# Kernel optimization log

Measured on AMD Instinct MI355X. Metric: run time of the kernel, lower is better.

The kernel has to match this reference:

```python
import jax, jax.numpy as jnp
import numpy as np

THETA = 10.0      # spike threshold
TAU_SR = 1.0      # SRM (psp) kernel time constant
TAU_REF = 1.0     # refractory kernel time constant
SCALE_REF = 2.0   # refractory kernel scale (SLAYER default: -2*theta peak)


@jax.custom_vjp
def spike_fn(v):
    # Heaviside on (membrane - theta); surrogate gradient in bwd (SLAYER-style pdf)
    return (v >= 0.0).astype(v.dtype)

def _spike_fwd(v):
    return spike_fn(v), v

def _spike_bwd(v, g):
    return (g * jnp.exp(-jnp.abs(v) / THETA) / THETA,)

spike_fn.defvjp(_spike_fwd, _spike_bwd)


def alpha_psp(x, tau):
    """Causal conv of x (T, B, F) with alpha kernel eps[k] = (k/tau)*exp(1-k/tau),
    implemented as a 2-state linear recurrence (exact for the discrete kernel)."""
    d = jnp.float32(np.exp(-1.0 / tau))
    c = jnp.float32(np.e / tau)

    def step(carry, xt):
        p, q = carry
        q = d * (q + p)          # q[t] = sum_s x[s]*(t-s)*d^(t-s)
        p = d * p + xt           # p[t] = sum_s x[s]*d^(t-s)
        return (p, q), c * q

    z = jnp.zeros_like(x[0])
    _, out = jax.lax.scan(step, (z, z), x)
    return out


def spike_dyn(u, tau_ref, scale_ref, theta):
    """Threshold-with-refractory dynamics. u: (T, B, F) synaptic drive.
    membrane[t] = u[t] - scale_ref*theta * (alpha refractory conv of past spikes)."""
    d = jnp.float32(np.exp(-1.0 / tau_ref))
    c = jnp.float32(np.e / tau_ref)
    cref = jnp.float32(-scale_ref * theta) * c

    def step(carry, ut):
        p, q = carry
        q = d * (q + p)                       # refractory trace (lag-0 coeff is 0)
        s = spike_fn(ut + cref * q - theta)   # spike if membrane >= theta
        p = d * p + s
        return (p, q), s

    z = jnp.zeros_like(u[0])
    _, s = jax.lax.scan(step, (z, z), u)
    return s


def setup_inputs() -> dict:
    key = jax.random.key(0)
    k1, k2, k3 = jax.random.split(key, 3)
    # sparse binary input spike trains, (B, C, H, W, T) SLAYER layout
    downsampled = (jax.random.uniform(k1, (16, 2, 50, 63, 500)) < 0.1).astype(jnp.float32)
    w1 = jax.random.normal(k2, (1024, 6300), dtype=jnp.float32) * 0.1
    w2 = jax.random.normal(k3, (20, 1024), dtype=jnp.float32) * 0.1
    return {"downsampled": downsampled, "w1": w1, "w2": w2}


def reference(downsampled, w1, w2):
    B, T = downsampled.shape[0], downsampled.shape[-1]
    x = downsampled.reshape(B, -1, T).transpose(2, 0, 1)   # (T, B, 6300)
    p1 = alpha_psp(x, TAU_SR)                              # psp filter
    u1 = jnp.einsum('tbf,of->tbo', p1, w1)                 # fc1 (per-timestep dense)
    s1 = spike_dyn(u1, TAU_REF, SCALE_REF, THETA)          # spike layer 1
    p2 = alpha_psp(s1, TAU_SR)
    u2 = jnp.einsum('tbh,oh->tbo', p2, w2)                 # fc2
    s2 = spike_dyn(u2, TAU_REF, SCALE_REF, THETA)
    return s2.transpose(1, 2, 0)                           # (B, output_size, T)
```

## Files before the change

### kernel.cpp

```cpp
#include <hip/hip_runtime.h>
#include <cstdint>
#include <cstddef>

#define T_N   500
#define B_N   16
#define F_IN  6300
#define KW    198
#define KPAD  6336
#define H1    1024
#define H2    20
#define N2P   32
#define M_N   8000
#define M_PADN 8064

#define DD_C   0.36787944117144233f
#define CC_C   2.718281828459045f
#define THETA_C 10.0f
#define INV2048 4.8828125e-4f

typedef _Float16 half8 __attribute__((ext_vector_type(8)));
typedef __attribute__((ext_vector_type(4))) float f32x4;

__device__ __forceinline__ unsigned short f2h_bits(float x) {
    union { _Float16 h; unsigned short u; } c; c.h = (_Float16)x; return c.u;
}
__device__ __forceinline__ float h2f(unsigned short u) {
    union { _Float16 h; unsigned short u; } c; c.u = u; return (float)c.h;
}

__global__ void prep_fused_k(const float* __restrict__ x,
                             const float* __restrict__ w1,
                             const float* __restrict__ w2,
                             uint32_t* __restrict__ bits_t,
                             unsigned short* __restrict__ w1f,
                             unsigned short* __restrict__ w2f) {
    const int bid = blockIdx.x;
    if (bid < 6336) {
        const int b    = bid & 15;
        const int tmp  = bid >> 4;
        const int w    = tmp % 198;
        const int tch2 = tmp / 198;
        const int t    = tch2 * 256 + threadIdx.x;
        if (t >= 504) return;
        const int m = t * 16 + b;
        uint32_t word = 0u;
        if (t < T_N) {
            const int fbase = w * 32;
            #pragma unroll
            for (int j = 0; j < 32; ++j) {
                const int f = fbase + j;
                float v = 0.f;
                if (f < F_IN) v = x[((size_t)b * F_IN + f) * T_N + t];
                word |= (v != 0.f ? 1u : 0u) << j;
            }
        }
        bits_t[(size_t)w * M_PADN + m] = word;
    } else if (bid < 6336 + 1024) {
        const int o = bid - 6336;
        #pragma unroll 1
        for (int it = 0; it < 25; ++it) {
            const int f = it * 256 + threadIdx.x;
            if (f >= KPAD) break;
            float w = (f < F_IN) ? w1[(size_t)o * F_IN + f] : 0.f;
            const unsigned short h1 = f2h_bits(w);
            const float r1 = w - h2f(h1);
            const unsigned short h2 = f2h_bits(r1 * 2048.0f);
            const size_t base = (size_t)o * KPAD + f;
            w1f[base]                     = h1;
            w1f[(size_t)H1 * KPAD + base] = h2;
        }
    } else {
        const int o = bid - 7360;
        #pragma unroll
        for (int it = 0; it < 4; ++it) {
            const int k = it * 256 + threadIdx.x;
            float w = (o < H2) ? w2[(size_t)o * H1 + k] : 0.f;
            const unsigned short h1 = f2h_bits(w);
            const float r1 = w - h2f(h1);
            const unsigned short h2 = f2h_bits(r1 * 2048.0f);
            const size_t base = (size_t)o * H1 + k;
            w2f[base]                    = h1;
            w2f[(size_t)N2P * H1 + base] = h2;
        }
    }
}

__global__ __launch_bounds__(256, 2)
void gemm1_mfma_k(const uint32_t* __restrict__ bits_t,
                  const unsigned short* __restrict__ w1f,
                  float* __restrict__ u1) {
    __shared__ uint32_t BsU[2][2 * 128 * 16];

    const int tid  = threadIdx.x;
    const int lane = tid & 63;
    const int wave = tid >> 6;
    const int wr = wave >> 1, wc = wave & 1;
    const int n0 = blockIdx.x * 128;
    const int m0 = blockIdx.y * 128;
    const int l15 = lane & 15, g = lane >> 4;

    const unsigned short* bsrc0 =
        w1f + (size_t)(n0 + (lane >> 2)) * KPAD + ((lane & 3) ^ ((lane >> 3) & 3)) * 8;

    const uint32_t* pbits = bits_t + m0 + wr * 64 + l15;

    f32x4 acc[2][4][4];
    const f32x4 fz = {0.f, 0.f, 0.f, 0.f};
    #pragma unroll
    for (int t = 0; t < 2; ++t)
        #pragma unroll
        for (int i = 0; i < 4; ++i)
            #pragma unroll
            for (int j = 0; j < 4; ++j) acc[t][i][j] = fz;

    int boff[4];
    #pragma unroll
    for (int ni = 0; ni < 4; ++ni) {
        const int br = wc * 64 + ni * 16 + l15;
        boff[ni] = br * 16 + ((g ^ ((br >> 1) & 3)) << 2);
    }

#define STAGE_B(tt, bb)                                                        \
    {                                                                          \
        _Pragma("unroll")                                                      \
        for (int j = 0; j < 4; ++j) {                                          \
            const int e    = wave * 4 + j;                                     \
            const int term = e >> 3;                                           \
            const int ii   = e & 7;                                            \
            const unsigned short* src =                                        \
                bsrc0 + (size_t)(term * H1 + ii * 16) * KPAD + (size_t)(tt) * 32; \
            __builtin_amdgcn_global_load_lds(                                  \
                (const __attribute__((address_space(1))) uint32_t*)src,        \
                (__attribute__((address_space(3))) uint32_t*)&BsU[bb][term * 2048 + ii * 256], \
                16, 0, 0);                                                     \
        }                                                                      \
    }

#define LOAD_W(W, tt)                                                          \
    {                                                                          \
        _Pragma("unroll")                                                      \
        for (int mi = 0; mi < 4; ++mi)                                         \
            W[mi] = pbits[(size_t)(tt) * M_PADN + mi * 16];                    \
    }

#define COMPUTE(W, bb)                                                         \
    {                                                                          \
        half8 af[4];                                                           \
        _Pragma("unroll")                                                      \
        for (int mi = 0; mi < 4; ++mi) {                                       \
            union { uint32_t u[4]; half8 h; } cv;                              \
            _Pragma("unroll")                                                  \
            for (int i = 0; i < 4; ++i) {                                      \
                const int b0 = g * 8 + 2 * i;                                  \
                cv.u[i] = (((W[mi] >> b0) & 1u) ? 0x00003C00u : 0u) |          \
                          (((W[mi] >> (b0 + 1)) & 1u) ? 0x3C000000u : 0u);     \
            }                                                                  \
            af[mi] = cv.h;                                                     \
        }                                                                      \
        __builtin_amdgcn_s_setprio(1);                                         \
        _Pragma("unroll")                                                      \
        for (int term = 0; term < 2; ++term) {                                 \
            half8 bfv[4];                                                      \
            _Pragma("unroll")                                                  \
            for (int ni = 0; ni < 4; ++ni)                                     \
                bfv[ni] = *(const half8*)&BsU[bb][term * 2048 + boff[ni]];     \
            _Pragma("unroll")                                                  \
            for (int mi = 0; mi < 4; ++mi)                                     \
                _Pragma("unroll")                                              \
                for (int ni = 0; ni < 4; ++ni)                                 \
                    acc[term][mi][ni] = __builtin_amdgcn_mfma_f32_16x16x32_f16( \
                        af[mi], bfv[ni], acc[term][mi][ni], 0, 0, 0);          \
        }                                                                      \
        __builtin_amdgcn_s_setprio(0);                                         \
    }

#define ITER(tt, cb, WCUR, WNEXT)                                              \
    {                                                                          \
        LOAD_W(WNEXT, (tt) + 1);                                               \
        STAGE_B((tt) + 1, (cb) ^ 1);                                           \
        COMPUTE(WCUR, cb);                                                     \
        __syncthreads();                                                       \
    }

    uint32_t wA[4], wB[4];
    LOAD_W(wA, 0);
    STAGE_B(0, 0);
    __syncthreads();

    for (int t = 0; t < KW - 2; t += 2) {
        ITER(t,     0, wA, wB);
        ITER(t + 1, 1, wB, wA);
    }
    ITER(KW - 2, 0, wA, wB);
    COMPUTE(wB, 1);

#undef ITER
#undef COMPUTE
#undef LOAD_W
#undef STAGE_B

    #pragma unroll
    for (int mi = 0; mi < 4; ++mi) {
        const int mbase = m0 + wr * 64 + mi * 16 + g * 4;
        #pragma unroll
        for (int ni = 0; ni < 4; ++ni) {
            const int o = n0 + wc * 64 + ni * 16 + l15;
            #pragma unroll
            for (int r = 0; r < 4; ++r)
                u1[(size_t)(mbase + r) * H1 + o] =
                    acc[0][mi][ni][r] + acc[1][mi][ni][r] * INV2048;
        }
    }
}

__global__ void scan1_k(const float* __restrict__ u1, unsigned short* __restrict__ s1f) {
    const int lane = blockIdx.x * 64 + threadIdx.x;
    const float CREF = -20.0f * CC_C;
    float p1 = 0.f, q1 = 0.f, pr = 0.f, qr = 0.f;
    float A[10], Bv[10];

#define STEP1(xv, tidx) {                                   \
        q1 = DD_C * (q1 + p1); p1 = DD_C * p1 + (xv);       \
        const float uu = CC_C * q1;                         \
        qr = DD_C * (qr + pr);                              \
        const float vv = uu + CREF * qr - THETA_C;          \
        const float ss = (vv >= 0.f) ? 1.f : 0.f;           \
        pr = DD_C * pr + ss;                                \
        s1f[(size_t)(tidx) * 16384 + lane] =                \
            (vv >= 0.f) ? (unsigned short)0x3C00 : (unsigned short)0; }

    #pragma unroll
    for (int j = 0; j < 10; ++j) A[j] = u1[(size_t)j * 16384 + lane];
    for (int it = 0; it < 25; ++it) {
        const int gB = 2 * it + 1;
        #pragma unroll
        for (int j = 0; j < 10; ++j) Bv[j] = u1[(size_t)(gB * 10 + j) * 16384 + lane];
        #pragma unroll
        for (int j = 0; j < 10; ++j) STEP1(A[j], (2 * it) * 10 + j);
        if (it < 24) {
            const int gA = 2 * it + 2;
            #pragma unroll
            for (int j = 0; j < 10; ++j) A[j] = u1[(size_t)(gA * 10 + j) * 16384 + lane];
        }
        #pragma unroll
        for (int j = 0; j < 10; ++j) STEP1(Bv[j], gB * 10 + j);
    }
#undef STEP1
}

__global__ __launch_bounds__(256)
void gemm2_mfma_k(const unsigned short* __restrict__ s1f,
                  const unsigned short* __restrict__ w2f,
                  float* __restrict__ u2p) {
    __shared__ uint32_t AsU[128 * 16];
    __shared__ uint32_t BsU[2 * 32 * 16];

    const int tid  = threadIdx.x;
    const int lane = tid & 63;
    const int wave = tid >> 6;
    const int m0 = blockIdx.x * 128;
    const int kc = blockIdx.y;
    const int l15 = lane & 15, g = lane >> 4;

    f32x4 acc[2][2][2];
    const f32x4 fz = {0.f, 0.f, 0.f, 0.f};
    #pragma unroll
    for (int t = 0; t < 2; ++t)
        #pragma unroll
        for (int i = 0; i < 2; ++i)
            #pragma unroll
            for (int j = 0; j < 2; ++j) acc[t][i][j] = fz;

    int aoff[2], boff[2][2];
    #pragma unroll
    for (int mi = 0; mi < 2; ++mi) {
        const int ar = wave * 32 + mi * 16 + l15;
        aoff[mi] = ar * 16 + ((g ^ ((ar >> 1) & 3)) << 2);
    }
    #pragma unroll
    for (int term = 0; term < 2; ++term)
        #pragma unroll
        for (int ni = 0; ni < 2; ++ni) {
            const int br = ni * 16 + l15;
            boff[term][ni] = term * 512 + br * 16 + ((g ^ ((br >> 1) & 3)) << 2);
        }

    for (int kw8 = 0; kw8 < 8; ++kw8) {
        const int kw = kc * 8 + kw8;
        __syncthreads();
        #pragma unroll
        for (int i = 0; i < 2; ++i) {
            const int c   = i * 256 + tid;
            const int row = c >> 2;
            const int kch = c & 3;
            const unsigned short* src =
                s1f + (size_t)(m0 + row) * H1 + kw * 32 + (kch ^ ((row >> 1) & 3)) * 8;
            __builtin_amdgcn_global_load_lds(
                (const __attribute__((address_space(1))) uint32_t*)src,
                (__attribute__((address_space(3))) uint32_t*)&AsU[(i * 256 + wave * 64) * 4],
                16, 0, 0);
        }
        {
            const int c    = tid;
            const int term = c >> 7;
            const int o    = (c >> 2) & 31;
            const int kch  = c & 3;
            const unsigned short* src =
                w2f + (size_t)(term * N2P + o) * H1 + kw * 32 + (kch ^ ((o >> 1) & 3)) * 8;
            __builtin_amdgcn_global_load_lds(
                (const __attribute__((address_space(1))) uint32_t*)src,
                (__attribute__((address_space(3))) uint32_t*)&BsU[wave * 256],
                16, 0, 0);
        }
        __syncthreads();

        half8 af[2];
        #pragma unroll
        for (int mi = 0; mi < 2; ++mi) af[mi] = *(const half8*)&AsU[aoff[mi]];
        #pragma unroll
        for (int term = 0; term < 2; ++term)
            #pragma unroll
            for (int ni = 0; ni < 2; ++ni) {
                const half8 bf = *(const half8*)&BsU[boff[term][ni]];
                #pragma unroll
                for (int mi = 0; mi < 2; ++mi)
                    acc[term][mi][ni] = __builtin_amdgcn_mfma_f32_16x16x32_f16(
                        af[mi], bf, acc[term][mi][ni], 0, 0, 0);
            }
    }

    #pragma unroll
    for (int mi = 0; mi < 2; ++mi) {
        const int mbase = m0 + wave * 32 + mi * 16 + g * 4;
        #pragma unroll
        for (int ni = 0; ni < 2; ++ni) {
            const int o = ni * 16 + l15;
            #pragma unroll
            for (int r = 0; r < 4; ++r)
                u2p[((size_t)kc * M_PADN + mbase + r) * N2P + o] =
                    acc[0][mi][ni][r] + acc[1][mi][ni][r] * INV2048;
        }
    }
}

__global__ void scan2_k(const float* __restrict__ u2p, float* __restrict__ out) {
    const int lane = blockIdx.x * 64 + threadIdx.x;
    if (lane >= 320) return;
    const int b  = lane / 20;
    const int o2 = lane % 20;
    const int boffs = b * N2P + o2;
    const float CREF = -20.0f * CC_C;
    float p1 = 0.f, q1 = 0.f, pr = 0.f, qr = 0.f;
    float A[10], Bv[10];

#define LOAD2(tidx)                                                         \
    (u2p[(size_t)0 * M_PADN * N2P + (size_t)(tidx) * 512 + boffs] +         \
     u2p[(size_t)1 * M_PADN * N2P + (size_t)(tidx) * 512 + boffs] +         \
     u2p[(size_t)2 * M_PADN * N2P + (size_t)(tidx) * 512 + boffs] +         \
     u2p[(size_t)3 * M_PADN * N2P + (size_t)(tidx) * 512 + boffs])

#define STEP2(xv, tidx) {                                   \
        q1 = DD_C * (q1 + p1); p1 = DD_C * p1 + (xv);       \
        const float uu = CC_C * q1;                         \
        qr = DD_C * (qr + pr);                              \
        const float vv = uu + CREF * qr - THETA_C;          \
        const float ss = (vv >= 0.f) ? 1.f : 0.f;           \
        pr = DD_C * pr + ss;                                \
        out[(size_t)lane * T_N + (tidx)] = ss; }

    #pragma unroll
    for (int j = 0; j < 10; ++j) A[j] = LOAD2(j);
    for (int it = 0; it < 25; ++it) {
        const int gB = 2 * it + 1;
        #pragma unroll
        for (int j = 0; j < 10; ++j) Bv[j] = LOAD2(gB * 10 + j);
        #pragma unroll
        for (int j = 0; j < 10; ++j) STEP2(A[j], (2 * it) * 10 + j);
        if (it < 24) {
            const int gA = 2 * it + 2;
            #pragma unroll
            for (int j = 0; j < 10; ++j) A[j] = LOAD2(gA * 10 + j);
        }
        #pragma unroll
        for (int j = 0; j < 10; ++j) STEP2(Bv[j], gB * 10 + j);
    }
#undef STEP2
#undef LOAD2
}

extern "C" void kernel_launch(void* const* d_in, const int* in_sizes, int n_in,
                              void* d_out, int out_size, void* d_ws, size_t ws_size,
                              hipStream_t stream) {
    const float* x  = (const float*)d_in[0];
    const float* w1 = (const float*)d_in[1];
    const float* w2 = (const float*)d_in[2];
    float* out = (float*)d_out;

    char* ws = (char*)d_ws;
    size_t off = 0;
    uint32_t*       bits_t = (uint32_t*)(ws + off);       off += (size_t)KW * M_PADN * 4;
    unsigned short* w1f    = (unsigned short*)(ws + off); off += (size_t)2 * H1 * KPAD * 2;
    unsigned short* w2f    = (unsigned short*)(ws + off); off += (size_t)2 * N2P * H1 * 2;
    float*          u1     = (float*)(ws + off);          off += (size_t)M_PADN * H1 * 4;
    unsigned short* s1f    = (unsigned short*)(ws + off); off += (size_t)M_PADN * H1 * 2;
    float*          u2p    = (float*)(ws + off);          off += (size_t)4 * M_PADN * N2P * 4;
    (void)ws_size; (void)in_sizes; (void)n_in; (void)out_size;

    prep_fused_k  <<<7392,        256, 0, stream>>>(x, w1, w2, bits_t, w1f, w2f);
    gemm1_mfma_k  <<<dim3(8, 63), 256, 0, stream>>>(bits_t, w1f, u1);
    scan1_k       <<<256,         64,  0, stream>>>(u1, s1f);
    gemm2_mfma_k  <<<dim3(63, 4), 256, 0, stream>>>(s1f, w2f, u2p);
    scan2_k       <<<5,           64,  0, stream>>>(u2p, out);
}
```

Baseline: 349.1 us.

## Replace split-fp16 GEMM1 with three-plane int8 MFMA on binary spike inputs

GEMM1 previously multiplied binary spike masks by a two-term fp16 split of w1 using f16 MFMA. Now w1 is quantized into three int8 planes (scales 2^-7, 2^-14, 2^-21) and multiplied with 0/1 int8 activations using the i32 16x16x64 i8 MFMA, so each instruction covers twice the K depth. Activation bits are unpacked with a multiply-and-mask trick, and the spike bit words are re-laid out in pairs so one uint2 load covers a 64-wide K step. The wave tiling changes to 8x2 tiles per wave. The cost is a third weight plane and a different quantization error profile, which the thresholded spike output is sensitive to.

```diff
diff --git a/kernel.cpp b/kernel.cpp
--- a/kernel.cpp
+++ b/kernel.cpp
@@ -6,6 +6,7 @@
 #define B_N   16
 #define F_IN  6300
 #define KW    198
+#define NS64  99
 #define KPAD  6336
 #define H1    1024
 #define H2    20
@@ -18,8 +19,13 @@
 #define THETA_C 10.0f
 #define INV2048 4.8828125e-4f
 
+#define S1_C 0.0078125f
+#define S2_C 6.103515625e-5f
+#define S3_C 4.76837158203125e-7f
+
 typedef _Float16 half8 __attribute__((ext_vector_type(8)));
 typedef __attribute__((ext_vector_type(4))) float f32x4;
+typedef __attribute__((ext_vector_type(4))) int   i32x4;
 
 __device__ __forceinline__ unsigned short f2h_bits(float x) {
     union { _Float16 h; unsigned short u; } c; c.h = (_Float16)x; return c.u;
@@ -31,8 +37,8 @@
 __global__ void prep_fused_k(const float* __restrict__ x,
                              const float* __restrict__ w1,
                              const float* __restrict__ w2,
-                             uint32_t* __restrict__ bits_t,
-                             unsigned short* __restrict__ w1f,
+                             uint32_t* __restrict__ bits2,
+                             signed char* __restrict__ w1q,
                              unsigned short* __restrict__ w2f) {
     const int bid = blockIdx.x;
     if (bid < 6336) {
@@ -54,7 +60,7 @@
                 word |= (v != 0.f ? 1u : 0u) << j;
             }
         }
-        bits_t[(size_t)w * M_PADN + m] = word;
+        bits2[(size_t)(w >> 1) * (M_PADN * 2) + m * 2 + (w & 1)] = word;
     } else if (bid < 6336 + 1024) {
         const int o = bid - 6336;
         #pragma unroll 1
@@ -62,12 +68,16 @@
             const int f = it * 256 + threadIdx.x;
             if (f >= KPAD) break;
             float w = (f < F_IN) ? w1[(size_t)o * F_IN + f] : 0.f;
-            const unsigned short h1 = f2h_bits(w);
-            const float r1 = w - h2f(h1);
-            const unsigned short h2 = f2h_bits(r1 * 2048.0f);
+            const int q1 = __float2int_rn(w * 128.0f);
+            const float r1 = w - (float)q1 * S1_C;
+            const int q2 = __float2int_rn(r1 * 16384.0f);
+            const float r2 = r1 - (float)q2 * S2_C;
+            const int q3 = __float2int_rn(r2 * 2097152.0f);
             const size_t base = (size_t)o * KPAD + f;
-            w1f[base]                     = h1;
-            w1f[(size_t)H1 * KPAD + base] = h2;
+            const size_t PL = (size_t)H1 * KPAD;
+            w1q[base]          = (signed char)q1;
+            w1q[PL + base]     = (signed char)q2;
+            w1q[2 * PL + base] = (signed char)q3;
         }
     } else {
         const int o = bid - 7360;
@@ -86,129 +96,115 @@
 }
 
 __global__ __launch_bounds__(256, 2)
-void gemm1_mfma_k(const uint32_t* __restrict__ bits_t,
-                  const unsigned short* __restrict__ w1f,
-                  float* __restrict__ u1) {
-    __shared__ uint32_t BsU[2][2 * 128 * 16];
+void gemm1_i8_k(const uint32_t* __restrict__ bits2,
+                const signed char* __restrict__ w1q,
+                float* __restrict__ u1) {
+    __shared__ uint32_t BsU[2][12 * 512];
 
     const int tid  = threadIdx.x;
     const int lane = tid & 63;
     const int wave = tid >> 6;
-    const int wr = wave >> 1, wc = wave & 1;
     const int n0 = blockIdx.x * 128;
     const int m0 = blockIdx.y * 128;
     const int l15 = lane & 15, g = lane >> 4;
 
-    const unsigned short* bsrc0 =
-        w1f + (size_t)(n0 + (lane >> 2)) * KPAD + ((lane & 3) ^ ((lane >> 3) & 3)) * 8;
-
-    const uint32_t* pbits = bits_t + m0 + wr * 64 + l15;
-
-    f32x4 acc[2][4][4];
-    const f32x4 fz = {0.f, 0.f, 0.f, 0.f};
-    #pragma unroll
-    for (int t = 0; t < 2; ++t)
-        #pragma unroll
-        for (int i = 0; i < 4; ++i)
-            #pragma unroll
-            for (int j = 0; j < 4; ++j) acc[t][i][j] = fz;
-
-    int boff[4];
-    #pragma unroll
-    for (int ni = 0; ni < 4; ++ni) {
-        const int br = wc * 64 + ni * 16 + l15;
-        boff[ni] = br * 16 + ((g ^ ((br >> 1) & 3)) << 2);
-    }
-
-#define STAGE_B(tt, bb)                                                        \
+    const signed char* bbase = w1q + (size_t)(n0 + lane) * KPAD;
+    uint32_t boffg[6];
+    uint32_t bdst[6];
+    #pragma unroll
+    for (int j = 0; j < 6; ++j) {
+        const int e = wave * 6 + j, slab = e >> 1, h = e & 1;
+        const int t = slab >> 2, gg = slab & 3;
+        boffg[j] = (uint32_t)((t * H1 + h * 64) * KPAD + gg * 16);
+        bdst[j]  = (uint32_t)(slab * 512 + h * 256 + lane * 4);
+    }
+
+    const uint2* pb = (const uint2*)bits2 + (size_t)m0 + l15;
+    const uint32_t hi2 = (g & 2);
+    const uint32_t sh  = (g & 1) * 16;
+
+    uint32_t bfoff[6];
+    #pragma unroll
+    for (int t = 0; t < 3; ++t)
+        #pragma unroll
+        for (int ni = 0; ni < 2; ++ni)
+            bfoff[t * 2 + ni] = (uint32_t)((t * 4 + g) * 512 + (wave * 32 + ni * 16 + l15) * 4);
+
+    i32x4 acc[3][8][2];
+    #pragma unroll
+    for (int t = 0; t < 3; ++t)
+        #pragma unroll
+        for (int mi = 0; mi < 8; ++mi)
+            #pragma unroll
+            for (int ni = 0; ni < 2; ++ni) acc[t][mi][ni] = (i32x4){0, 0, 0, 0};
+
+#define STAGE(ss, bb)                                                          \
     {                                                                          \
         _Pragma("unroll")                                                      \
-        for (int j = 0; j < 4; ++j) {                                          \
-            const int e    = wave * 4 + j;                                     \
-            const int term = e >> 3;                                           \
-            const int ii   = e & 7;                                            \
-            const unsigned short* src =                                        \
-                bsrc0 + (size_t)(term * H1 + ii * 16) * KPAD + (size_t)(tt) * 32; \
+        for (int j = 0; j < 6; ++j) {                                          \
             __builtin_amdgcn_global_load_lds(                                  \
-                (const __attribute__((address_space(1))) uint32_t*)src,        \
-                (__attribute__((address_space(3))) uint32_t*)&BsU[bb][term * 2048 + ii * 256], \
+                (const __attribute__((address_space(1))) uint32_t*)            \
+                    (bbase + (size_t)boffg[j] + (size_t)(ss) * 64),            \
+                (__attribute__((address_space(3))) uint32_t*)&BsU[bb][bdst[j]],\
                 16, 0, 0);                                                     \
         }                                                                      \
     }
 
-#define LOAD_W(W, tt)                                                          \
-    {                                                                          \
-        _Pragma("unroll")                                                      \
-        for (int mi = 0; mi < 4; ++mi)                                         \
-            W[mi] = pbits[(size_t)(tt) * M_PADN + mi * 16];                    \
-    }
-
-#define COMPUTE(W, bb)                                                         \
-    {                                                                          \
-        half8 af[4];                                                           \
-        _Pragma("unroll")                                                      \
-        for (int mi = 0; mi < 4; ++mi) {                                       \
-            union { uint32_t u[4]; half8 h; } cv;                              \
-            _Pragma("unroll")                                                  \
-            for (int i = 0; i < 4; ++i) {                                      \
-                const int b0 = g * 8 + 2 * i;                                  \
-                cv.u[i] = (((W[mi] >> b0) & 1u) ? 0x00003C00u : 0u) |          \
-                          (((W[mi] >> (b0 + 1)) & 1u) ? 0x3C000000u : 0u);     \
-            }                                                                  \
-            af[mi] = cv.h;                                                     \
-        }                                                                      \
-        __builtin_amdgcn_s_setprio(1);                                         \
-        _Pragma("unroll")                                                      \
-        for (int term = 0; term < 2; ++term) {                                 \
-            half8 bfv[4];                                                      \
-            _Pragma("unroll")                                                  \
-            for (int ni = 0; ni < 4; ++ni)                                     \
-                bfv[ni] = *(const half8*)&BsU[bb][term * 2048 + boff[ni]];     \
-            _Pragma("unroll")                                                  \
-            for (int mi = 0; mi < 4; ++mi)                                     \
-                _Pragma("unroll")                                              \
-                for (int ni = 0; ni < 4; ++ni)                                 \
-                    acc[term][mi][ni] = __builtin_amdgcn_mfma_f32_16x16x32_f16( \
-                        af[mi], bfv[ni], acc[term][mi][ni], 0, 0, 0);          \
-        }                                                                      \
-        __builtin_amdgcn_s_setprio(0);                                         \
-    }
-
-#define ITER(tt, cb, WCUR, WNEXT)                                              \
-    {                                                                          \
-        LOAD_W(WNEXT, (tt) + 1);                                               \
-        STAGE_B((tt) + 1, (cb) ^ 1);                                           \
-        COMPUTE(WCUR, cb);                                                     \
-        __syncthreads();                                                       \
-    }
-
-    uint32_t wA[4], wB[4];
-    LOAD_W(wA, 0);
-    STAGE_B(0, 0);
+    const uint32_t MAGIC = 0x00204081u;
+    const uint32_t PICK  = 0x01010101u;
+
+    STAGE(0, 0);
     __syncthreads();
 
-    for (int t = 0; t < KW - 2; t += 2) {
-        ITER(t,     0, wA, wB);
-        ITER(t + 1, 1, wB, wA);
-    }
-    ITER(KW - 2, 0, wA, wB);
-    COMPUTE(wB, 1);
-
-#undef ITER
-#undef COMPUTE
-#undef LOAD_W
-#undef STAGE_B
-
-    #pragma unroll
-    for (int mi = 0; mi < 4; ++mi) {
-        const int mbase = m0 + wr * 64 + mi * 16 + g * 4;
-        #pragma unroll
-        for (int ni = 0; ni < 4; ++ni) {
-            const int o = n0 + wc * 64 + ni * 16 + l15;
-            #pragma unroll
-            for (int r = 0; r < 4; ++r)
-                u1[(size_t)(mbase + r) * H1 + o] =
-                    acc[0][mi][ni][r] + acc[1][mi][ni][r] * INV2048;
+    for (int step = 0; step < NS64; ++step) {
+        const int cur = step & 1;
+        uint2 Wv[8];
+        const uint2* pbs = pb + (size_t)step * M_PADN;
+        #pragma unroll
+        for (int mi = 0; mi < 8; ++mi) Wv[mi] = pbs[mi * 16];
+        if (step < NS64 - 1) STAGE(step + 1, cur ^ 1);
+        i32x4 bf[3][2];
+        {
+            const uint32_t cbase = (uint32_t)cur * (12 * 512);
+            #pragma unroll
+            for (int t = 0; t < 3; ++t)
+                #pragma unroll
+                for (int ni = 0; ni < 2; ++ni)
+                    bf[t][ni] = *(const i32x4*)&BsU[0][cbase + bfoff[t * 2 + ni]];
+        }
+        __builtin_amdgcn_s_setprio(1);
+        #pragma unroll
+        for (int mi = 0; mi < 8; ++mi) {
+            const uint32_t sel = hi2 ? Wv[mi].y : Wv[mi].x;
+            i32x4 af;
+            #pragma unroll
+            for (int jj = 0; jj < 4; ++jj)
+                af[jj] = (int)((((sel >> (sh + 4 * jj)) & 0xFu) * MAGIC) & PICK);
+            #pragma unroll
+            for (int t = 0; t < 3; ++t)
+                #pragma unroll
+                for (int ni = 0; ni < 2; ++ni)
+                    acc[t][mi][ni] = __builtin_amdgcn_mfma_i32_16x16x64_i8(
+                        af, bf[t][ni], acc[t][mi][ni], 0, 0, 0);
+        }
+        __builtin_amdgcn_s_setprio(0);
+        __syncthreads();
+    }
+#undef STAGE
+
+    #pragma unroll
+    for (int mi = 0; mi < 8; ++mi) {
+        const int mbase = m0 + mi * 16 + g * 4;
+        #pragma unroll
+        for (int ni = 0; ni < 2; ++ni) {
+            const int o = n0 + wave * 32 + ni * 16 + l15;
+            #pragma unroll
+            for (int r = 0; r < 4; ++r) {
+                const float v = fmaf(S1_C, (float)acc[0][mi][ni][r],
+                              fmaf(S2_C, (float)acc[1][mi][ni][r],
+                                   S3_C * (float)acc[2][mi][ni][r]));
+                u1[(size_t)(mbase + r) * H1 + o] = v;
+            }
         }
     }
 }
@@ -398,17 +394,17 @@
 
     char* ws = (char*)d_ws;
     size_t off = 0;
-    uint32_t*       bits_t = (uint32_t*)(ws + off);       off += (size_t)KW * M_PADN * 4;
-    unsigned short* w1f    = (unsigned short*)(ws + off); off += (size_t)2 * H1 * KPAD * 2;
-    unsigned short* w2f    = (unsigned short*)(ws + off); off += (size_t)2 * N2P * H1 * 2;
-    float*          u1     = (float*)(ws + off);          off += (size_t)M_PADN * H1 * 4;
-    unsigned short* s1f    = (unsigned short*)(ws + off); off += (size_t)M_PADN * H1 * 2;
-    float*          u2p    = (float*)(ws + off);          off += (size_t)4 * M_PADN * N2P * 4;
+    uint32_t*       bits2 = (uint32_t*)(ws + off);       off += (size_t)NS64 * M_PADN * 8;
+    signed char*    w1q   = (signed char*)(ws + off);    off += (size_t)3 * H1 * KPAD;
+    unsigned short* w2f   = (unsigned short*)(ws + off); off += (size_t)2 * N2P * H1 * 2;
+    float*          u1    = (float*)(ws + off);          off += (size_t)M_PADN * H1 * 4;
+    unsigned short* s1f   = (unsigned short*)(ws + off); off += (size_t)M_PADN * H1 * 2;
+    float*          u2p   = (float*)(ws + off);          off += (size_t)4 * M_PADN * N2P * 4;
     (void)ws_size; (void)in_sizes; (void)n_in; (void)out_size;
 
-    prep_fused_k  <<<7392,        256, 0, stream>>>(x, w1, w2, bits_t, w1f, w2f);
-    gemm1_mfma_k  <<<dim3(8, 63), 256, 0, stream>>>(bits_t, w1f, u1);
-    scan1_k       <<<256,         64,  0, stream>>>(u1, s1f);
-    gemm2_mfma_k  <<<dim3(63, 4), 256, 0, stream>>>(s1f, w2f, u2p);
-    scan2_k       <<<5,           64,  0, stream>>>(u2p, out);
-}
+    prep_fused_k <<<7392,        256, 0, stream>>>(x, w1, w2, bits2, w1q, w2f);
+    gemm1_i8_k   <<<dim3(8, 63), 256, 0, stream>>>(bits2, w1q, u1);
+    scan1_k      <<<256,         64,  0, stream>>>(u1, s1f);
+    gemm2_mfma_k <<<dim3(63, 4), 256, 0, stream>>>(s1f, w2f, u2p);
+    scan2_k      <<<5,           64,  0, stream>>>(u2p, out);
+}
```

After: 600.8 us. 72.1% more time.
